# Performance work log

Measured on AMD Instinct MI355X. Metric: run time of the kernel, lower is better.

The kernel has to match this reference:

```python
import jax, jax.numpy as jnp
import numpy as np

N_NODES = 50000
N_EDGES = 800000
D_IN = 128
D_OUT = 128


def _gcn_conv(x, W, b, src, dst, num_nodes):
    """PyG GCNConv: h = x @ W^T; symmetric-normalized mean over neighbors
    (with self-loops); out = aggregate + bias.
    src/dst already include self-loops."""
    h = x @ W.T  # [N, C_out]
    ones = jnp.ones(dst.shape[0], dtype=x.dtype)
    deg = jax.ops.segment_sum(ones, dst, num_segments=num_nodes)  # in-degree incl self-loop
    deg_inv_sqrt = jnp.where(deg > 0, jax.lax.rsqrt(deg), 0.0)
    norm = deg_inv_sqrt[src] * deg_inv_sqrt[dst]  # [E+N]
    msgs = h[src] * norm[:, None]  # gather + scale
    out = jax.ops.segment_sum(msgs, dst, num_segments=num_nodes)  # scatter-add
    return out + b


def setup_inputs() -> dict:
    key = jax.random.key(0)
    ks = jax.random.split(key, 9)
    x_r1 = jax.random.normal(ks[0], (N_NODES, D_IN), dtype=jnp.float32)
    x_r2 = jax.random.normal(ks[1], (N_NODES, D_IN), dtype=jnp.float32)
    x_i1 = jax.random.normal(ks[2], (N_NODES, D_IN), dtype=jnp.float32)
    x_i2 = jax.random.normal(ks[3], (N_NODES, D_IN), dtype=jnp.float32)
    edge_index = jax.random.randint(ks[4], (2, N_EDGES), 0, N_NODES, dtype=jnp.int64)
    s = 1.0 / np.sqrt(D_IN)
    W1 = jax.random.uniform(ks[5], (D_OUT, D_IN), minval=-s, maxval=s, dtype=jnp.float32)
    W2 = jax.random.uniform(ks[6], (D_OUT, D_IN), minval=-s, maxval=s, dtype=jnp.float32)
    b1 = jax.random.uniform(ks[7], (D_OUT,), minval=-s, maxval=s, dtype=jnp.float32)
    b2 = jax.random.uniform(ks[8], (D_OUT,), minval=-s, maxval=s, dtype=jnp.float32)
    return {"x_r1": x_r1, "x_r2": x_r2, "x_i1": x_i1, "x_i2": x_i2,
            "edge_index": edge_index, "W1": W1, "b1": b1, "W2": W2, "b2": b2}


def reference(x_r1, x_r2, x_i1, x_i2, edge_index, W1, b1, W2, b2):
    num_nodes = x_r1.shape[0]
    loops = jnp.arange(num_nodes, dtype=edge_index.dtype)
    src = jnp.concatenate([edge_index[0], loops])  # add self-loops
    dst = jnp.concatenate([edge_index[1], loops])
    # real1/imag1 share (W1, b1); real2/imag2 share (W2, b2)
    h_r1 = _gcn_conv(x_r1, W1, b1, src, dst, num_nodes)
    h_r2 = _gcn_conv(x_r2, W2, b2, src, dst, num_nodes)
    h_i1 = _gcn_conv(x_i1, W1, b1, src, dst, num_nodes)
    h_i2 = _gcn_conv(x_i2, W2, b2, src, dst, num_nodes)
    return (h_r1, h_r2, h_i1, h_i2)
```

## Files before the change

### kernel.cpp

```cpp
#include <hip/hip_runtime.h>

#define DD 128

typedef __bf16 bf16x8 __attribute__((ext_vector_type(8)));
typedef float f32x4 __attribute__((ext_vector_type(4)));

static __device__ __forceinline__ unsigned short f2bf(float f) {
    unsigned int u = __float_as_uint(f);
    u += 0x7FFF + ((u >> 16) & 1);
    return (unsigned short)(u >> 16);
}


__global__ void k_count(const int* __restrict__ dst, int* __restrict__ cnt, int E) {
    int e4 = (blockIdx.x * 256 + threadIdx.x) * 4;
    if (e4 < E) {
        int4 d = *(const int4*)&dst[e4];
        atomicAdd(&cnt[d.x], 1); atomicAdd(&cnt[d.y], 1);
        atomicAdd(&cnt[d.z], 1); atomicAdd(&cnt[d.w], 1);
    }
}

__global__ __launch_bounds__(1024) void k_scan1(const int* __restrict__ cnt,
                                                int* __restrict__ rp,
                                                float* __restrict__ dinv,
                                                int* __restrict__ bsum,
                                                const float* __restrict__ W1,
                                                const float* __restrict__ W2,
                                                unsigned short* __restrict__ wbf,
                                                int N, int nscan) {
    const int bid = blockIdx.x;
    if (bid >= nscan) {
        int i = (bid - nscan) * 1024 + threadIdx.x;
        float4 v = (i < 4096) ? ((const float4*)W1)[i] : ((const float4*)W2)[i - 4096];
        ushort4 b;
        b.x = f2bf(v.x); b.y = f2bf(v.y); b.z = f2bf(v.z); b.w = f2bf(v.w);
        *(ushort4*)&wbf[(size_t)i * 4] = b;
        return;
    }
    __shared__ int wsum[16];
    const int tid = threadIdx.x, lane = tid & 63, wid = tid >> 6;
    const int i = bid * 1024 + tid;
    int v = (i < N) ? cnt[i] : 0;
    int s = v;
    for (int off = 1; off < 64; off <<= 1) {
        int t = __shfl_up(s, off, 64);
        if (lane >= off) s += t;
    }
    if (lane == 63) wsum[wid] = s;
    __syncthreads();
    int woff = 0, total = 0;
#pragma unroll
    for (int w2 = 0; w2 < 16; ++w2) {
        int t = wsum[w2];
        if (w2 < wid) woff += t;
        total += t;
    }
    if (i < N) {
        rp[i + 1] = woff + s;
        dinv[i] = rsqrtf((float)(v + 1));
    }
    if (tid == 0) bsum[bid] = total;
}

__global__ __launch_bounds__(1024) void k_scan2(const int* __restrict__ bsum,
                                                int* __restrict__ rp, int N) {
    __shared__ int boff_s;
    const int tid = threadIdx.x;
    if (tid < 64) {
        int v = (tid < (int)blockIdx.x) ? bsum[tid] : 0;
        for (int off = 32; off > 0; off >>= 1) v += __shfl_down(v, off, 64);
        if (tid == 0) boff_s = v;
    }
    __syncthreads();
    const int i = blockIdx.x * 1024 + tid;
    if (i < N) rp[i + 1] += boff_s;
    if (i == 0) rp[0] = 0;
}

__global__ void k_fill(const int* __restrict__ ei, const int* __restrict__ rp,
                       int* __restrict__ cnt, const float* __restrict__ dinv,
                       int2* __restrict__ csr, int E) {
    int e2 = (blockIdx.x * 256 + threadIdx.x) * 2;
    if (e2 >= E) return;
    int2 s = *(const int2*)&ei[e2];
    int2 d = *(const int2*)&ei[E + e2];
    int o0 = atomicSub(&cnt[d.x], 1);
    csr[rp[d.x] + o0 - 1] = make_int2(s.x, __float_as_int(dinv[s.x]));
    int o1 = atomicSub(&cnt[d.y], 1);
    csr[rp[d.y] + o1 - 1] = make_int2(s.y, __float_as_int(dinv[s.y]));
}


__global__ __launch_bounds__(512) void k_gemm(
    const float* __restrict__ x0, const float* __restrict__ x1,
    const float* __restrict__ x2, const float* __restrict__ x3,
    const unsigned short* __restrict__ wbf,
    unsigned short* __restrict__ h, int N)
{
    const int m = blockIdx.y;
    const float* x = (m == 0) ? x0 : (m == 1) ? x1 : (m == 2) ? x2 : x3;
    const unsigned short* Wg = wbf + (size_t)(m & 1) * 128 * 128;

    __shared__ unsigned short Ws[128 * 128];
    __shared__ unsigned short ts[128 * 136];

    const int tid = threadIdx.x;
    const int n0 = blockIdx.x * 128;

#pragma unroll
    for (int t = tid; t < 2048; t += 512)
        ((uint4*)Ws)[t ^ ((t >> 4) & 7)] = ((const uint4*)Wg)[t];
    for (int t = tid; t < 128 * 32; t += 512) {
        int r = t >> 5;
        int n = n0 + r;
        float4 v = make_float4(0.f, 0.f, 0.f, 0.f);
        if (n < N) v = ((const float4*)(x + (size_t)n * DD))[t & 31];
        ushort4 b;
        b.x = f2bf(v.x); b.y = f2bf(v.y); b.z = f2bf(v.z); b.w = f2bf(v.w);
        *(ushort4*)&ts[r * 128 + (((t & 31) * 4) ^ ((r & 7) << 3))] = b;
    }
    __syncthreads();

    const int w    = tid >> 6;
    const int lane = tid & 63;
    const int am   = lane & 15;
    const int aq   = lane >> 4;
    const int r0   = w * 16;

    f32x4 acc[8] = {};
#pragma unroll
    for (int kk = 0; kk < 128; kk += 32) {
        const int ar = r0 + am;
        bf16x8 af = *(const bf16x8*)&ts[ar * 128 + ((kk + aq * 8) ^ ((ar & 7) << 3))];
#pragma unroll
        for (int ct = 0; ct < 8; ++ct) {
            bf16x8 bf = *(const bf16x8*)&Ws[(ct * 16 + am) * 128 +
                                            ((kk + aq * 8) ^ ((am & 7) << 3))];
            acc[ct] = __builtin_amdgcn_mfma_f32_16x16x32_bf16(af, bf, acc[ct], 0, 0, 0);
        }
    }
    __syncthreads();

    const int cc = lane & 15;
    const int rr = (lane >> 4) * 4;
#pragma unroll
    for (int ct = 0; ct < 8; ++ct)
#pragma unroll
        for (int i = 0; i < 4; ++i)
            ts[(r0 + rr + i) * 136 + ct * 16 + cc] = f2bf(acc[ct][i]);
    __syncthreads();

#pragma unroll
    for (int k = 0; k < 4; ++k) {
        int f = k * 512 + tid;
        int row = f >> 4, ch = f & 15;
        int n = n0 + row;
        if (n < N) {
            uint4 v = *(const uint4*)&ts[row * 136 + ch * 8];
            *(uint4*)(h + ((size_t)n * 4 + m) * DD + ch * 8) = v;
        }
    }
}


static __device__ __forceinline__ void acc8(float* a, uint4 v, float wt) {
    a[0] += __uint_as_float(v.x << 16) * wt;
    a[1] += __uint_as_float(v.x & 0xffff0000u) * wt;
    a[2] += __uint_as_float(v.y << 16) * wt;
    a[3] += __uint_as_float(v.y & 0xffff0000u) * wt;
    a[4] += __uint_as_float(v.z << 16) * wt;
    a[5] += __uint_as_float(v.z & 0xffff0000u) * wt;
    a[6] += __uint_as_float(v.w << 16) * wt;
    a[7] += __uint_as_float(v.w & 0xffff0000u) * wt;
}

__global__ __launch_bounds__(256) void k_gather(
    const int* __restrict__ rp, const int2* __restrict__ csr,
    const float* __restrict__ dinv, const unsigned short* __restrict__ h,
    const float* __restrict__ b1, const float* __restrict__ b2,
    float* __restrict__ out, int N)
{
    const int n = blockIdx.x * 4 + (threadIdx.x >> 6);
    if (n >= N) return;
    const int lane = threadIdx.x & 63;
    const int m    = lane >> 4;
    const int c    = (lane & 15) * 8;
    const size_t off = (size_t)lane * 8;

    const float dn = dinv[n];
    float a[8];

    {
        const float sn = dn * dn;
        const float* bb = (m & 1) ? b2 : b1;
        uint4 hv = *(const uint4*)(h + (size_t)n * 512 + off);
        float4 bv0 = *(const float4*)(bb + c);
        float4 bv1 = *(const float4*)(bb + c + 4);
        a[0] = bv0.x; a[1] = bv0.y; a[2] = bv0.z; a[3] = bv0.w;
        a[4] = bv1.x; a[5] = bv1.y; a[6] = bv1.z; a[7] = bv1.w;
        acc8(a, hv, sn);
    }

    int jb = rp[n];
    const int j1 = rp[n + 1];

    for (; jb + 3 < j1; jb += 4) {
        int2 e0 = csr[jb], e1 = csr[jb + 1], e2 = csr[jb + 2], e3 = csr[jb + 3];
        float w0 = __int_as_float(e0.y) * dn, w1 = __int_as_float(e1.y) * dn,
              w2 = __int_as_float(e2.y) * dn, w3 = __int_as_float(e3.y) * dn;
        uint4 v0 = *(const uint4*)(h + (size_t)e0.x * 512 + off);
        uint4 v1 = *(const uint4*)(h + (size_t)e1.x * 512 + off);
        uint4 v2 = *(const uint4*)(h + (size_t)e2.x * 512 + off);
        uint4 v3 = *(const uint4*)(h + (size_t)e3.x * 512 + off);
        acc8(a, v0, w0); acc8(a, v1, w1); acc8(a, v2, w2); acc8(a, v3, w3);
    }
    for (; jb < j1; ++jb) {
        int2 e = csr[jb];
        float wt = __int_as_float(e.y) * dn;
        uint4 v = *(const uint4*)(h + (size_t)e.x * 512 + off);
        acc8(a, v, wt);
    }

    float* po = out + ((size_t)m * N + n) * DD + c;
    f32x4 r0, r1;
    r0.x = a[0]; r0.y = a[1]; r0.z = a[2]; r0.w = a[3];
    r1.x = a[4]; r1.y = a[5]; r1.z = a[6]; r1.w = a[7];
    __builtin_nontemporal_store(r0, (f32x4*)po);
    __builtin_nontemporal_store(r1, (f32x4*)(po + 4));
}


extern "C" void kernel_launch(void* const* d_in, const int* in_sizes, int n_in,
                              void* d_out, int out_size, void* d_ws, size_t ws_size,
                              hipStream_t stream) {
    const float* x0 = (const float*)d_in[0];
    const float* x1 = (const float*)d_in[1];
    const float* x2 = (const float*)d_in[2];
    const float* x3 = (const float*)d_in[3];
    const int*   ei = (const int*)d_in[4];
    const float* W1 = (const float*)d_in[5];
    const float* b1 = (const float*)d_in[6];
    const float* W2 = (const float*)d_in[7];
    const float* b2 = (const float*)d_in[8];
    float* out = (float*)d_out;

    const int N = in_sizes[0] / DD;
    const int E = in_sizes[4] / 2;

    int*   cnt  = (int*)d_ws;
    int*   rp   = cnt + 65536;
    float* dinv = (float*)(rp + 65536);
    int*   bsum = (int*)(dinv + 65536);
    unsigned short* wbf = (unsigned short*)(bsum + 256);
    int2*  csr  = (int2*)(wbf + 2 * 128 * 128);
    unsigned short* h = (unsigned short*)(csr + E);

    const int nscan = (N + 1023) / 1024;

    hipMemsetAsync(cnt, 0, (size_t)N * sizeof(int), stream);
    k_count<<<(E / 4 + 255) / 256, 256, 0, stream>>>(ei + E, cnt, E);
    k_scan1<<<nscan + 8, 1024, 0, stream>>>(cnt, rp, dinv, bsum, W1, W2, wbf, N, nscan);
    k_scan2<<<nscan, 1024, 0, stream>>>(bsum, rp, N);
    k_fill <<<(E / 2 + 255) / 256, 256, 0, stream>>>(ei, rp, cnt, dinv, csr, E);

    dim3 g((N + 127) / 128, 4);
    k_gemm<<<g, 512, 0, stream>>>(x0, x1, x2, x3, wbf, h, N);

    k_gather<<<(N + 3) / 4, 256, 0, stream>>>(rp, csr, dinv, h, b1, b2, out, N);
}
```

Baseline: 418.8 us.

## Load GEMM A fragments directly to registers, halve epilogue LDS, unroll gather by 8

```diff
diff --git a/kernel.cpp b/kernel.cpp
--- a/kernel.cpp
+++ b/kernel.cpp
@@ -103,63 +103,88 @@
     const unsigned short* Wg = wbf + (size_t)(m & 1) * 128 * 128;
 
     __shared__ unsigned short Ws[128 * 128];
-    __shared__ unsigned short ts[128 * 136];
-
-    const int tid = threadIdx.x;
-    const int n0 = blockIdx.x * 128;
-
-#pragma unroll
-    for (int t = tid; t < 2048; t += 512)
-        ((uint4*)Ws)[t ^ ((t >> 4) & 7)] = ((const uint4*)Wg)[t];
-    for (int t = tid; t < 128 * 32; t += 512) {
-        int r = t >> 5;
-        int n = n0 + r;
-        float4 v = make_float4(0.f, 0.f, 0.f, 0.f);
-        if (n < N) v = ((const float4*)(x + (size_t)n * DD))[t & 31];
-        ushort4 b;
-        b.x = f2bf(v.x); b.y = f2bf(v.y); b.z = f2bf(v.z); b.w = f2bf(v.w);
-        *(ushort4*)&ts[r * 128 + (((t & 31) * 4) ^ ((r & 7) << 3))] = b;
-    }
-    __syncthreads();
-
+    __shared__ unsigned short eb[64 * 136];
+
+    const int tid  = threadIdx.x;
+    const int n0   = blockIdx.x * 128;
     const int w    = tid >> 6;
     const int lane = tid & 63;
     const int am   = lane & 15;
     const int aq   = lane >> 4;
     const int r0   = w * 16;
 
+    int arow = n0 + r0 + am; if (arow > N - 1) arow = N - 1;
+    const float* xr = x + (size_t)arow * DD + aq * 8;
+    float4 a0[4], a1[4];
+#pragma unroll
+    for (int q = 0; q < 4; ++q) {
+        a0[q] = *(const float4*)(xr + q * 32);
+        a1[q] = *(const float4*)(xr + q * 32 + 4);
+    }
+
+#pragma unroll
+    for (int t = tid; t < 2048; t += 512)
+        ((uint4*)Ws)[t ^ ((t >> 4) & 7)] = ((const uint4*)Wg)[t];
+    __syncthreads();
+
+    bf16x8 afr[4];
+#pragma unroll
+    for (int q = 0; q < 4; ++q) {
+        afr[q][0] = (__bf16)a0[q].x; afr[q][1] = (__bf16)a0[q].y;
+        afr[q][2] = (__bf16)a0[q].z; afr[q][3] = (__bf16)a0[q].w;
+        afr[q][4] = (__bf16)a1[q].x; afr[q][5] = (__bf16)a1[q].y;
+        afr[q][6] = (__bf16)a1[q].z; afr[q][7] = (__bf16)a1[q].w;
+    }
+
     f32x4 acc[8] = {};
 #pragma unroll
-    for (int kk = 0; kk < 128; kk += 32) {
-        const int ar = r0 + am;
-        bf16x8 af = *(const bf16x8*)&ts[ar * 128 + ((kk + aq * 8) ^ ((ar & 7) << 3))];
+    for (int q = 0; q < 4; ++q) {
+        const int kc = q * 32 + aq * 8;
 #pragma unroll
         for (int ct = 0; ct < 8; ++ct) {
             bf16x8 bf = *(const bf16x8*)&Ws[(ct * 16 + am) * 128 +
-                                            ((kk + aq * 8) ^ ((am & 7) << 3))];
-            acc[ct] = __builtin_amdgcn_mfma_f32_16x16x32_bf16(af, bf, acc[ct], 0, 0, 0);
+                                            (kc ^ ((am & 7) << 3))];
+            acc[ct] = __builtin_amdgcn_mfma_f32_16x16x32_bf16(afr[q], bf, acc[ct], 0, 0, 0);
         }
     }
-    __syncthreads();
 
     const int cc = lane & 15;
     const int rr = (lane >> 4) * 4;
-#pragma unroll
-    for (int ct = 0; ct < 8; ++ct)
-#pragma unroll
-        for (int i = 0; i < 4; ++i)
-            ts[(r0 + rr + i) * 136 + ct * 16 + cc] = f2bf(acc[ct][i]);
-    __syncthreads();
-
-#pragma unroll
-    for (int k = 0; k < 4; ++k) {
+
+    if (w < 4) {
+#pragma unroll
+        for (int ct = 0; ct < 8; ++ct)
+#pragma unroll
+            for (int i = 0; i < 4; ++i)
+                eb[(r0 + rr + i) * 136 + ct * 16 + cc] = f2bf(acc[ct][i]);
+    }
+    __syncthreads();
+#pragma unroll
+    for (int k = 0; k < 2; ++k) {
         int f = k * 512 + tid;
-        int row = f >> 4, ch = f & 15;
-        int n = n0 + row;
-        if (n < N) {
-            uint4 v = *(const uint4*)&ts[row * 136 + ch * 8];
-            *(uint4*)(h + ((size_t)n * 4 + m) * DD + ch * 8) = v;
-        }
+        int row2 = f >> 4, ch = f & 15;
+        int n = n0 + row2;
+        if (n < N)
+            *(uint4*)(h + ((size_t)n * 4 + m) * DD + ch * 8) =
+                *(const uint4*)&eb[row2 * 136 + ch * 8];
+    }
+    __syncthreads();
+    if (w >= 4) {
+#pragma unroll
+        for (int ct = 0; ct < 8; ++ct)
+#pragma unroll
+            for (int i = 0; i < 4; ++i)
+                eb[(r0 - 64 + rr + i) * 136 + ct * 16 + cc] = f2bf(acc[ct][i]);
+    }
+    __syncthreads();
+#pragma unroll
+    for (int k = 0; k < 2; ++k) {
+        int f = k * 512 + tid;
+        int row2 = f >> 4, ch = f & 15;
+        int n = n0 + 64 + row2;
+        if (n < N)
+            *(uint4*)(h + ((size_t)n * 4 + m) * DD + ch * 8) =
+                *(const uint4*)&eb[row2 * 136 + ch * 8];
     }
 }
 
@@ -205,21 +230,34 @@
     int jb = rp[n];
     const int j1 = rp[n + 1];
 
-    for (; jb + 3 < j1; jb += 4) {
-        int2 e0 = csr[jb], e1 = csr[jb + 1], e2 = csr[jb + 2], e3 = csr[jb + 3];
+    for (; jb + 7 < j1; jb += 8) {
+        int2 e0 = csr[jb],     e1 = csr[jb + 1], e2 = csr[jb + 2], e3 = csr[jb + 3];
+        int2 e4 = csr[jb + 4], e5 = csr[jb + 5], e6 = csr[jb + 6], e7 = csr[jb + 7];
         float w0 = __int_as_float(e0.y) * dn, w1 = __int_as_float(e1.y) * dn,
-              w2 = __int_as_float(e2.y) * dn, w3 = __int_as_float(e3.y) * dn;
+              w2 = __int_as_float(e2.y) * dn, w3 = __int_as_float(e3.y) * dn,
+              w4 = __int_as_float(e4.y) * dn, w5 = __int_as_float(e5.y) * dn,
+              w6 = __int_as_float(e6.y) * dn, w7 = __int_as_float(e7.y) * dn;
         uint4 v0 = *(const uint4*)(h + (size_t)e0.x * 512 + off);
         uint4 v1 = *(const uint4*)(h + (size_t)e1.x * 512 + off);
         uint4 v2 = *(const uint4*)(h + (size_t)e2.x * 512 + off);
         uint4 v3 = *(const uint4*)(h + (size_t)e3.x * 512 + off);
+        uint4 v4 = *(const uint4*)(h + (size_t)e4.x * 512 + off);
+        uint4 v5 = *(const uint4*)(h + (size_t)e5.x * 512 + off);
+        uint4 v6 = *(const uint4*)(h + (size_t)e6.x * 512 + off);
+        uint4 v7 = *(const uint4*)(h + (size_t)e7.x * 512 + off);
         acc8(a, v0, w0); acc8(a, v1, w1); acc8(a, v2, w2); acc8(a, v3, w3);
-    }
-    for (; jb < j1; ++jb) {
-        int2 e = csr[jb];
-        float wt = __int_as_float(e.y) * dn;
-        uint4 v = *(const uint4*)(h + (size_t)e.x * 512 + off);
-        acc8(a, v, wt);
+        acc8(a, v4, w4); acc8(a, v5, w5); acc8(a, v6, w6); acc8(a, v7, w7);
+    }
+    if (jb < j1) {
+        const int last = j1 - 1;
+#pragma unroll
+        for (int k = 0; k < 8; ++k) {
+            int idx = jb + k;
+            int2 e = csr[idx <= last ? idx : last];
+            float wt = (idx <= last) ? __int_as_float(e.y) * dn : 0.f;
+            uint4 v = *(const uint4*)(h + (size_t)e.x * 512 + off);
+            acc8(a, v, wt);
+        }
     }
 
     float* po = out + ((size_t)m * N + n) * DD + c;
```

Measured after the change: 405.1 us. 3.3% less time.
